# Kernel tuning notes

Hardware: AMD Instinct MI355X
Metric: run time of the kernel (lower is better)

The kernel has to match this reference:

```python
import jax, jax.numpy as jnp
import numpy as np

N, D, H = 50000, 256, 8
HD = D // H
E = 800000
NEG_SLOPE = 0.2


def setup_inputs() -> dict:
    key = jax.random.key(0)
    ks = jax.random.split(key, 12)
    s = 1.0 / np.sqrt(D)
    return {
        "x": jax.random.normal(ks[0], (N, D), jnp.float32),
        "edge_index": jax.random.randint(ks[1], (2, E), 0, N, jnp.int64),
        "edge_attr": jax.random.normal(ks[2], (E, 16), jnp.float32),
        # GATConv params: lin weight (no bias), attention vectors, output bias
        "W": jax.random.normal(ks[3], (D, D), jnp.float32) * s,
        "att_src": jax.random.normal(ks[4], (H, HD), jnp.float32) * s,
        "att_dst": jax.random.normal(ks[5], (H, HD), jnp.float32) * s,
        "bias": jnp.zeros((D,), jnp.float32),
        # LayerNorm
        "ln_g": jnp.ones((D,), jnp.float32),
        "ln_b": jnp.zeros((D,), jnp.float32),
        # FFN
        "W1": jax.random.normal(ks[6], (D, D), jnp.float32) * s,
        "b1": jnp.zeros((D,), jnp.float32),
        "W2": jax.random.normal(ks[7], (D, D), jnp.float32) * s,
        "b2": jnp.zeros((D,), jnp.float32),
    }


def _gat_layer(x, edge_index, W, att_src, att_dst, bias, ln_g, ln_b, W1, b1, W2, b2):
    n = x.shape[0]
    # GATConv default add_self_loops=True
    sl = jnp.arange(n, dtype=edge_index.dtype)
    src = jnp.concatenate([edge_index[0], sl])  # [E+N]
    dst = jnp.concatenate([edge_index[1], sl])  # [E+N]

    xp = (x @ W).reshape(n, H, HD)                      # [N,H,hd]
    a_src = jnp.einsum("nhd,hd->nh", xp, att_src)        # [N,H]
    a_dst = jnp.einsum("nhd,hd->nh", xp, att_dst)        # [N,H]

    e = a_src[src] + a_dst[dst]                          # [E+N,H]
    e = jax.nn.leaky_relu(e, NEG_SLOPE)
    # segment softmax over destination nodes (every node has a self loop)
    m = jax.ops.segment_max(e, dst, num_segments=n)      # [N,H]
    ex = jnp.exp(e - m[dst])
    denom = jax.ops.segment_sum(ex, dst, num_segments=n) # [N,H]
    alpha = ex / (denom[dst] + 1e-16)                    # [E+N,H]

    msg = alpha[:, :, None] * xp[src]                    # [E+N,H,hd]
    out = jax.ops.segment_sum(msg, dst, num_segments=n)  # [N,H,hd]
    h = out.reshape(n, D) + bias

    # residual + LayerNorm
    r = h + x
    mu = jnp.mean(r, axis=-1, keepdims=True)
    var = jnp.mean(jnp.square(r - mu), axis=-1, keepdims=True)
    hn = (r - mu) / jnp.sqrt(var + 1e-5) * ln_g + ln_b

    # FFN
    return jax.nn.relu(hn @ W1 + b1) @ W2 + b2


def reference(x, edge_index, edge_attr, W, att_src, att_dst, bias, ln_g, ln_b, W1, b1, W2, b2):
    # edge_attr is accepted but unused (GATConv built without edge_dim)
    return _gat_layer(x, edge_index, W, att_src, att_dst, bias, ln_g, ln_b, W1, b1, W2, b2)
```

## Files before the change

### kernel.cpp

```cpp
#include <hip/hip_runtime.h>
#include <hip/hip_bf16.h>

#define H 8
#define HD 32
#define DD 256
#define NEG_SLOPE 0.2f

typedef short bf16x8 __attribute__((ext_vector_type(8)));
typedef float f32x4 __attribute__((ext_vector_type(4)));

__device__ __forceinline__ unsigned short f2bf(float f) {
    unsigned int u = __float_as_uint(f);
    unsigned int r = (u + 0x7fffu + ((u >> 16) & 1u)) >> 16;
    return (unsigned short)r;
}
__device__ __forceinline__ float bf2f(unsigned short b) {
    return __uint_as_float(((unsigned int)b) << 16);
}

#define GLOAD_LDS16(g, s)                                                        \
    __builtin_amdgcn_global_load_lds((const __attribute__((address_space(1))) void*)(g), \
                                     (__attribute__((address_space(3))) void*)(s), 16, 0, 0)

__global__ __launch_bounds__(256) void prep(const float* __restrict__ x, unsigned short* __restrict__ xb,
                                            const float* __restrict__ W, unsigned short* __restrict__ Wt,
                                            const float* __restrict__ W1, unsigned short* __restrict__ W1t,
                                            const float* __restrict__ W2, unsigned short* __restrict__ W2t,
                                            int* __restrict__ cnt, int N, int n4, int ZB) {
    int b = blockIdx.x;
    int tid = threadIdx.x;
    if (b < 768) {
        const float* src = (b < 256) ? W : (b < 512) ? W1 : W2;
        unsigned short* dst = (b < 256) ? Wt : (b < 512) ? W1t : W2t;
        int i = (b & 255) * 256 + tid;
        int n = i >> 8, k = i & 255;
        dst[i] = f2bf(src[k * 256 + n]);
    } else if (b < 768 + ZB) {
        int i = (b - 768) * 256 + tid;
        if (i < N) cnt[i] = 0;
    } else {
        int i = (b - 768 - ZB) * 256 + tid;
        if (i < n4) {
            float4 v = ((const float4*)x)[i];
            ushort4 o;
            o.x = f2bf(v.x); o.y = f2bf(v.y); o.z = f2bf(v.z); o.w = f2bf(v.w);
            ((ushort4*)xb)[i] = o;
        }
    }
}

template <bool ATTN, bool PHASE2>
__global__ __launch_bounds__(256) void gemm_fused(
    const unsigned short* __restrict__ A,
    const unsigned short* __restrict__ B1t, const float* __restrict__ b1,
    const unsigned short* __restrict__ B2t, const float* __restrict__ b2,
    void* __restrict__ Cout, int M,
    const float* __restrict__ att_s, const float* __restrict__ att_d,
    float* __restrict__ a_srcO, float* __restrict__ a_dstO) {
    __shared__ __align__(16) unsigned short Als[4096];
    __shared__ __align__(16) unsigned short Bls[16384];
    __shared__ __align__(16) unsigned short t1ls[PHASE2 ? 64 * 280 : 8];

    const int tid = threadIdx.x;
    const int l = tid & 63;
    const int w = tid >> 6;
    const int r16 = l & 15, q0 = l >> 4;
    const int row0 = blockIdx.x * 64;

    const int ca0 = w * 128 + l, ca1 = ca0 + 64;
    const unsigned short* gA0 = A + (size_t)min(row0 + (ca0 & 63), M - 1) * DD + (ca0 >> 6) * 8;
    const unsigned short* gA1 = A + (size_t)min(row0 + (ca1 & 63), M - 1) * DD + (ca1 >> 6) * 8;
    unsigned short* lA0 = &Als[ca0 * 8];
    unsigned short* lA1 = &Als[ca1 * 8];

    const unsigned short* gB[8];
    unsigned short* lB[8];
#pragma unroll
    for (int k = 0; k < 8; k++) {
        int c = w * 512 + k * 64 + l;
        gB[k] = B1t + (size_t)(c & 255) * DD + (c >> 8) * 8;
        lB[k] = &Bls[c * 8];
    }

    f32x4 zero = {0.f, 0.f, 0.f, 0.f};
    f32x4 acc[4][4];
#pragma unroll
    for (int i = 0; i < 4; i++)
#pragma unroll
        for (int j = 0; j < 4; j++) acc[i][j] = zero;

    for (int kk = 0; kk < 256; kk += 64) {
        GLOAD_LDS16(gA0 + kk, lA0);
        GLOAD_LDS16(gA1 + kk, lA1);
#pragma unroll
        for (int k = 0; k < 8; k++) GLOAD_LDS16(gB[k] + kk, lB[k]);
        __syncthreads();
#pragma unroll
        for (int t = 0; t < 2; t++) {
            int q = t * 4 + q0;
            bf16x8 af[4], bf[4];
#pragma unroll
            for (int i = 0; i < 4; i++)
                af[i] = *(const bf16x8*)&Als[(q * 64 + i * 16 + r16) * 8];
#pragma unroll
            for (int j = 0; j < 4; j++)
                bf[j] = *(const bf16x8*)&Bls[(q * 256 + w * 64 + j * 16 + r16) * 8];
#pragma unroll
            for (int i = 0; i < 4; i++)
#pragma unroll
                for (int j = 0; j < 4; j++)
                    acc[i][j] = __builtin_amdgcn_mfma_f32_16x16x32_bf16(af[i], bf[j], acc[i][j], 0, 0, 0);
        }
        __syncthreads();
    }

    if (!PHASE2) {
        float aws0, aws1, aws2, aws3, awd0, awd1, awd2, awd3;
        int hA = 0, hB = 0;
        if (ATTN) {
            hA = w * 2; hB = hA + 1;
            aws0 = att_s[hA * HD + r16];
            aws1 = att_s[hA * HD + 16 + r16];
            aws2 = att_s[hB * HD + r16];
            aws3 = att_s[hB * HD + 16 + r16];
            awd0 = att_d[hA * HD + r16];
            awd1 = att_d[hA * HD + 16 + r16];
            awd2 = att_d[hB * HD + r16];
            awd3 = att_d[hB * HD + 16 + r16];
        }
#pragma unroll
        for (int i = 0; i < 4; i++) {
#pragma unroll
            for (int r = 0; r < 4; r++) {
                int row = row0 + i * 16 + q0 * 4 + r;
                if (row < M) {
#pragma unroll
                    for (int j = 0; j < 4; j++) {
                        int col = w * 64 + j * 16 + r16;
                        ((unsigned short*)Cout)[(size_t)row * DD + col] = f2bf(acc[i][j][r]);
                    }
                }
                if (ATTN) {
                    float v0 = acc[i][0][r], v1 = acc[i][1][r];
                    float v2 = acc[i][2][r], v3 = acc[i][3][r];
                    float ps0 = v0 * aws0 + v1 * aws1;
                    float ps1 = v2 * aws2 + v3 * aws3;
                    float pd0 = v0 * awd0 + v1 * awd1;
                    float pd1 = v2 * awd2 + v3 * awd3;
#pragma unroll
                    for (int m = 1; m < 16; m <<= 1) {
                        ps0 += __shfl_xor(ps0, m, 64);
                        ps1 += __shfl_xor(ps1, m, 64);
                        pd0 += __shfl_xor(pd0, m, 64);
                        pd1 += __shfl_xor(pd1, m, 64);
                    }
                    if (r16 == 0 && row < M) {
                        a_srcO[row * H + hA] = ps0;
                        a_srcO[row * H + hB] = ps1;
                        a_dstO[row * H + hA] = pd0;
                        a_dstO[row * H + hB] = pd1;
                    }
                }
            }
        }
    } else {
        float bb1[4];
#pragma unroll
        for (int j = 0; j < 4; j++) bb1[j] = b1[w * 64 + j * 16 + r16];
#pragma unroll
        for (int i = 0; i < 4; i++)
#pragma unroll
            for (int r = 0; r < 4; r++) {
                int rl = i * 16 + q0 * 4 + r;
#pragma unroll
                for (int j = 0; j < 4; j++) {
                    float v = fmaxf(acc[i][j][r] + bb1[j], 0.f);
                    t1ls[rl * 280 + w * 64 + j * 16 + r16] = f2bf(v);
                }
            }
        __syncthreads();

        const unsigned short* gB2[8];
#pragma unroll
        for (int k = 0; k < 8; k++) {
            int c = w * 512 + k * 64 + l;
            gB2[k] = B2t + (size_t)(c & 255) * DD + (c >> 8) * 8;
        }
#pragma unroll
        for (int i = 0; i < 4; i++)
#pragma unroll
            for (int j = 0; j < 4; j++) acc[i][j] = zero;

        for (int kk = 0; kk < 256; kk += 64) {
#pragma unroll
            for (int k = 0; k < 8; k++) GLOAD_LDS16(gB2[k] + kk, lB[k]);
            __syncthreads();
#pragma unroll
            for (int t = 0; t < 2; t++) {
                int q = t * 4 + q0;
                bf16x8 af[4], bf[4];
#pragma unroll
                for (int i = 0; i < 4; i++)
                    af[i] = *(const bf16x8*)&t1ls[(i * 16 + r16) * 280 + kk + q * 8];
#pragma unroll
                for (int j = 0; j < 4; j++)
                    bf[j] = *(const bf16x8*)&Bls[(q * 256 + w * 64 + j * 16 + r16) * 8];
#pragma unroll
                for (int i = 0; i < 4; i++)
#pragma unroll
                    for (int j = 0; j < 4; j++)
                        acc[i][j] = __builtin_amdgcn_mfma_f32_16x16x32_bf16(af[i], bf[j], acc[i][j], 0, 0, 0);
            }
            __syncthreads();
        }

        float bb2[4];
#pragma unroll
        for (int j = 0; j < 4; j++) bb2[j] = b2[w * 64 + j * 16 + r16];
#pragma unroll
        for (int i = 0; i < 4; i++)
#pragma unroll
            for (int r = 0; r < 4; r++) {
                int row = row0 + i * 16 + q0 * 4 + r;
                if (row < M) {
#pragma unroll
                    for (int j = 0; j < 4; j++) {
                        int col = w * 64 + j * 16 + r16;
                        ((float*)Cout)[(size_t)row * DD + col] = acc[i][j][r] + bb2[j];
                    }
                }
            }
    }
}

__global__ void hist_kernel(const int* __restrict__ ei, int* __restrict__ counts, int E) {
    int e = blockIdx.x * blockDim.x + threadIdx.x;
    if (e < E) atomicAdd(&counts[ei[E + e]], 1);
}

__global__ __launch_bounds__(1024) void scan_block(const int* __restrict__ cnt,
                                                   int* __restrict__ row_ptr,
                                                   int* __restrict__ bsum, int N) {
    __shared__ int ws[16];
    int i = blockIdx.x * 1024 + threadIdx.x;
    int lane = threadIdx.x & 63, w = threadIdx.x >> 6;
    int v = (i < N) ? cnt[i] : 0;
    int sv = v;
#pragma unroll
    for (int off = 1; off < 64; off <<= 1) {
        int t = __shfl_up(sv, off, 64);
        if (lane >= off) sv += t;
    }
    if (lane == 63) ws[w] = sv;
    __syncthreads();
    if (w == 0) {
        int s = (lane < 16) ? ws[lane] : 0;
#pragma unroll
        for (int off = 1; off < 16; off <<= 1) {
            int t = __shfl_up(s, off, 64);
            if (lane >= off) s += t;
        }
        if (lane < 16) ws[lane] = s;
    }
    __syncthreads();
    int incl = sv + ((w > 0) ? ws[w - 1] : 0);
    if (i < N) row_ptr[i + 1] = incl;
    if (threadIdx.x == 1023) bsum[blockIdx.x] = incl;
}

__global__ void scan_partial(int* __restrict__ bsum, int nb) {
    int lane = threadIdx.x;
    int v = (lane < nb) ? bsum[lane] : 0;
    int s = v;
#pragma unroll
    for (int off = 1; off < 64; off <<= 1) {
        int t = __shfl_up(s, off, 64);
        if (lane >= off) s += t;
    }
    if (lane < nb) bsum[lane] = s - v;
}

__global__ __launch_bounds__(1024) void scan_add(int* __restrict__ row_ptr,
                                                 const int* __restrict__ bsum, int N) {
    int i = blockIdx.x * 1024 + threadIdx.x;
    if (i == 0) row_ptr[0] = 0;
    if (i < N) row_ptr[i + 1] += bsum[blockIdx.x];
}

__global__ void scatter_kernel(const int* __restrict__ ei, int* __restrict__ row_ptr,
                               int* __restrict__ src_sorted, int E) {
    int e = blockIdx.x * blockDim.x + threadIdx.x;
    if (e >= E) return;
    int s = ei[e];
    int d = ei[E + e];
    int pos = atomicAdd(&row_ptr[d], 1);
    src_sorted[pos] = s;
}

__global__ __launch_bounds__(256) void aggregate_ln(
    const unsigned short* __restrict__ xp, const unsigned short* __restrict__ x_bf,
    const float* __restrict__ a_src, const float* __restrict__ a_dst,
    const int* __restrict__ rp, const int* __restrict__ src_sorted,
    const float* __restrict__ bias, const float* __restrict__ ln_g,
    const float* __restrict__ ln_b, unsigned short* __restrict__ hn, int N) {
    int wave = threadIdx.x >> 6;
    int lane = threadIdx.x & 63;
    int n = blockIdx.x * 4 + wave;
    if (n >= N) return;
    int h = lane >> 3;

    float adst = a_dst[n * H + h];
    float e0 = a_src[n * H + h] + adst;
    e0 = (e0 > 0.f) ? e0 : NEG_SLOPE * e0;
    float ex = __expf(e0);
    ushort4 u = *(const ushort4*)(xp + (size_t)n * DD + lane * 4);
    float acc0 = ex * bf2f(u.x), acc1 = ex * bf2f(u.y);
    float acc2 = ex * bf2f(u.z), acc3 = ex * bf2f(u.w);
    float denom = ex;

    int beg = (n > 0) ? rp[n - 1] : 0;
    int end = rp[n];
    int i = beg;
    for (; i + 7 < end; i += 8) {
        int s[8];
        float es[8];
        ushort4 uu[8];
#pragma unroll
        for (int k = 0; k < 8; k++) s[k] = src_sorted[i + k];
#pragma unroll
        for (int k = 0; k < 8; k++) es[k] = a_src[s[k] * H + h];
#pragma unroll
        for (int k = 0; k < 8; k++) uu[k] = *(const ushort4*)(xp + (size_t)s[k] * DD + lane * 4);
#pragma unroll
        for (int k = 0; k < 8; k++) {
            float e = es[k] + adst;
            e = (e > 0.f) ? e : NEG_SLOPE * e;
            float wk = __expf(e);
            acc0 += wk * bf2f(uu[k].x);
            acc1 += wk * bf2f(uu[k].y);
            acc2 += wk * bf2f(uu[k].z);
            acc3 += wk * bf2f(uu[k].w);
            denom += wk;
        }
    }
    for (; i < end; i++) {
        int s0 = src_sorted[i];
        float es0 = a_src[s0 * H + h];
        ushort4 u0 = *(const ushort4*)(xp + (size_t)s0 * DD + lane * 4);
        float e0a = es0 + adst;
        e0a = (e0a > 0.f) ? e0a : NEG_SLOPE * e0a;
        float w0 = __expf(e0a);
        acc0 += w0 * bf2f(u0.x);
        acc1 += w0 * bf2f(u0.y);
        acc2 += w0 * bf2f(u0.z);
        acc3 += w0 * bf2f(u0.w);
        denom += w0;
    }
    float inv = 1.f / (denom + 1e-16f);
    float4 bb = *(const float4*)(bias + lane * 4);
    ushort4 xr = *(const ushort4*)(x_bf + (size_t)n * DD + lane * 4);
    float r0 = acc0 * inv + bb.x + bf2f(xr.x);
    float r1 = acc1 * inv + bb.y + bf2f(xr.y);
    float r2 = acc2 * inv + bb.z + bf2f(xr.z);
    float r3 = acc3 * inv + bb.w + bf2f(xr.w);

    float s = r0 + r1 + r2 + r3;
#pragma unroll
    for (int m = 1; m < 64; m <<= 1) s += __shfl_xor(s, m, 64);
    float mu = s * (1.f / 256.f);
    float d0 = r0 - mu, d1 = r1 - mu, d2 = r2 - mu, d3 = r3 - mu;
    float qv = d0 * d0 + d1 * d1 + d2 * d2 + d3 * d3;
#pragma unroll
    for (int m = 1; m < 64; m <<= 1) qv += __shfl_xor(qv, m, 64);
    float rstd = rsqrtf(qv * (1.f / 256.f) + 1e-5f);
    float4 g = *(const float4*)(ln_g + lane * 4);
    float4 b = *(const float4*)(ln_b + lane * 4);
    ushort4 o;
    o.x = f2bf(d0 * rstd * g.x + b.x);
    o.y = f2bf(d1 * rstd * g.y + b.y);
    o.z = f2bf(d2 * rstd * g.z + b.z);
    o.w = f2bf(d3 * rstd * g.w + b.w);
    *(ushort4*)(hn + (size_t)n * DD + lane * 4) = o;
}

extern "C" void kernel_launch(void* const* d_in, const int* in_sizes, int n_in,
                              void* d_out, int out_size, void* d_ws, size_t ws_size,
                              hipStream_t stream) {
    const float* x = (const float*)d_in[0];
    const int* edge_index = (const int*)d_in[1];
    const float* W = (const float*)d_in[3];
    const float* att_src = (const float*)d_in[4];
    const float* att_dst = (const float*)d_in[5];
    const float* bias = (const float*)d_in[6];
    const float* ln_g = (const float*)d_in[7];
    const float* ln_b = (const float*)d_in[8];
    const float* W1 = (const float*)d_in[9];
    const float* b1 = (const float*)d_in[10];
    const float* W2 = (const float*)d_in[11];
    const float* b2 = (const float*)d_in[12];

    const int N = in_sizes[0] / DD;
    const int E = in_sizes[1] / 2;

    char* p = (char*)d_ws;
    auto carve = [&](size_t bytes) {
        char* r = p;
        p += (bytes + 255) & ~(size_t)255;
        return r;
    };
    unsigned short* x_bf = (unsigned short*)carve((size_t)N * DD * 2);
    unsigned short* xp_bf = (unsigned short*)carve((size_t)N * DD * 2);
    unsigned short* hn_bf = (unsigned short*)carve((size_t)N * DD * 2);
    float* a_src = (float*)carve((size_t)N * H * 4);
    float* a_dst = (float*)carve((size_t)N * H * 4);
    int* row_ptr = (int*)carve((size_t)(N + 1) * 4);
    int* cnt = (int*)carve((size_t)N * 4);
    int* bsum = (int*)carve(256 * 4);
    int* src_sorted = (int*)carve((size_t)E * 4);
    unsigned short* Wt = (unsigned short*)carve(65536 * 2);
    unsigned short* W1t = (unsigned short*)carve(65536 * 2);
    unsigned short* W2t = (unsigned short*)carve(65536 * 2);

    const int n4 = N * DD / 4;
    const int ZB = (N + 255) / 256;

    int prep_blocks = 768 + ZB + (n4 + 255) / 256;
    prep<<<prep_blocks, 256, 0, stream>>>(x, x_bf, W, Wt, W1, W1t, W2, W2t, cnt, N, n4, ZB);

    const int gblocks = (N + 63) / 64;

    gemm_fused<true, false><<<gblocks, 256, 0, stream>>>(
        x_bf, Wt, nullptr, nullptr, nullptr, xp_bf, N, att_src, att_dst, a_src, a_dst);

    hist_kernel<<<(E + 255) / 256, 256, 0, stream>>>(edge_index, cnt, E);
    int nb = (N + 1023) / 1024;
    scan_block<<<nb, 1024, 0, stream>>>(cnt, row_ptr, bsum, N);
    scan_partial<<<1, 64, 0, stream>>>(bsum, nb);
    scan_add<<<nb, 1024, 0, stream>>>(row_ptr, bsum, N);
    scatter_kernel<<<(E + 255) / 256, 256, 0, stream>>>(edge_index, row_ptr, src_sorted, E);

    aggregate_ln<<<(N + 3) / 4, 256, 0, stream>>>(xp_bf, x_bf, a_src, a_dst, row_ptr, src_sorted,
                                                  bias, ln_g, ln_b, hn_bf, N);

    gemm_fused<false, true><<<gblocks, 256, 0, stream>>>(
        hn_bf, W1t, b1, W2t, b2, d_out, N, nullptr, nullptr, nullptr, nullptr);
}
```

Before: 396.8 us.

## Fuse CSR build into prep and GEMM kernels using per-edge ranks

The histogram now runs inside the prep kernel and records each edge's atomic rank within its destination. The scatter becomes a plain write at row_ptr[d]+rank, carried out by extra blocks appended to the first GEMM launch. The separate partial-scan kernel is folded into scan_add, which sums the block totals itself. This removes several kernel launches and the second pass of atomics, at the cost of an extra rank array in memory and a separate zeroing kernel.

```diff
diff --git a/kernel.cpp b/kernel.cpp
--- a/kernel.cpp
+++ b/kernel.cpp
@@ -22,11 +22,17 @@
     __builtin_amdgcn_global_load_lds((const __attribute__((address_space(1))) void*)(g), \
                                      (__attribute__((address_space(3))) void*)(s), 16, 0, 0)
 
+__global__ __launch_bounds__(256) void zero_cnt(int* __restrict__ cnt, int N) {
+    int i = blockIdx.x * 256 + threadIdx.x;
+    if (i < N) cnt[i] = 0;
+}
+
 __global__ __launch_bounds__(256) void prep(const float* __restrict__ x, unsigned short* __restrict__ xb,
                                             const float* __restrict__ W, unsigned short* __restrict__ Wt,
                                             const float* __restrict__ W1, unsigned short* __restrict__ W1t,
                                             const float* __restrict__ W2, unsigned short* __restrict__ W2t,
-                                            int* __restrict__ cnt, int N, int n4, int ZB) {
+                                            const int* __restrict__ ei, int* __restrict__ rank,
+                                            int* __restrict__ cnt, int N, int n4, int E, int HB) {
     int b = blockIdx.x;
     int tid = threadIdx.x;
     if (b < 768) {
@@ -35,11 +41,11 @@
         int i = (b & 255) * 256 + tid;
         int n = i >> 8, k = i & 255;
         dst[i] = f2bf(src[k * 256 + n]);
-    } else if (b < 768 + ZB) {
-        int i = (b - 768) * 256 + tid;
-        if (i < N) cnt[i] = 0;
+    } else if (b < 768 + HB) {
+        int e = (b - 768) * 256 + tid;
+        if (e < E) rank[e] = atomicAdd(&cnt[ei[E + e]], 1);
     } else {
-        int i = (b - 768 - ZB) * 256 + tid;
+        int i = (b - 768 - HB) * 256 + tid;
         if (i < n4) {
             float4 v = ((const float4*)x)[i];
             ushort4 o;
@@ -56,12 +62,27 @@
     const unsigned short* __restrict__ B2t, const float* __restrict__ b2,
     void* __restrict__ Cout, int M,
     const float* __restrict__ att_s, const float* __restrict__ att_d,
-    float* __restrict__ a_srcO, float* __restrict__ a_dstO) {
+    float* __restrict__ a_srcO, float* __restrict__ a_dstO,
+    const int* __restrict__ ei, const int* __restrict__ rank,
+    const int* __restrict__ rp, int* __restrict__ src_sorted, int E, int gB) {
     __shared__ __align__(16) unsigned short Als[4096];
     __shared__ __align__(16) unsigned short Bls[16384];
     __shared__ __align__(16) unsigned short t1ls[PHASE2 ? 64 * 280 : 8];
 
     const int tid = threadIdx.x;
+
+    if constexpr (ATTN) {
+        if ((int)blockIdx.x >= gB) {
+            int e = ((int)blockIdx.x - gB) * 256 + tid;
+            if (e < E) {
+                int s = ei[e];
+                int d = ei[E + e];
+                src_sorted[rp[d] + rank[e]] = s;
+            }
+            return;
+        }
+    }
+
     const int l = tid & 63;
     const int w = tid >> 6;
     const int r16 = l & 15, q0 = l >> 4;
@@ -73,12 +94,12 @@
     unsigned short* lA0 = &Als[ca0 * 8];
     unsigned short* lA1 = &Als[ca1 * 8];
 
-    const unsigned short* gB[8];
+    const unsigned short* gB8[8];
     unsigned short* lB[8];
 #pragma unroll
     for (int k = 0; k < 8; k++) {
         int c = w * 512 + k * 64 + l;
-        gB[k] = B1t + (size_t)(c & 255) * DD + (c >> 8) * 8;
+        gB8[k] = B1t + (size_t)(c & 255) * DD + (c >> 8) * 8;
         lB[k] = &Bls[c * 8];
     }
 
@@ -93,7 +114,7 @@
         GLOAD_LDS16(gA0 + kk, lA0);
         GLOAD_LDS16(gA1 + kk, lA1);
 #pragma unroll
-        for (int k = 0; k < 8; k++) GLOAD_LDS16(gB[k] + kk, lB[k]);
+        for (int k = 0; k < 8; k++) GLOAD_LDS16(gB8[k] + kk, lB[k]);
         __syncthreads();
 #pragma unroll
         for (int t = 0; t < 2; t++) {
@@ -233,11 +254,6 @@
     }
 }
 
-__global__ void hist_kernel(const int* __restrict__ ei, int* __restrict__ counts, int E) {
-    int e = blockIdx.x * blockDim.x + threadIdx.x;
-    if (e < E) atomicAdd(&counts[ei[E + e]], 1);
-}
-
 __global__ __launch_bounds__(1024) void scan_block(const int* __restrict__ cnt,
                                                    int* __restrict__ row_ptr,
                                                    int* __restrict__ bsum, int N) {
@@ -268,33 +284,22 @@
     if (threadIdx.x == 1023) bsum[blockIdx.x] = incl;
 }
 
-__global__ void scan_partial(int* __restrict__ bsum, int nb) {
-    int lane = threadIdx.x;
-    int v = (lane < nb) ? bsum[lane] : 0;
-    int s = v;
-#pragma unroll
-    for (int off = 1; off < 64; off <<= 1) {
-        int t = __shfl_up(s, off, 64);
-        if (lane >= off) s += t;
-    }
-    if (lane < nb) bsum[lane] = s - v;
-}
-
 __global__ __launch_bounds__(1024) void scan_add(int* __restrict__ row_ptr,
                                                  const int* __restrict__ bsum, int N) {
-    int i = blockIdx.x * 1024 + threadIdx.x;
+    __shared__ int offs;
+    int b = blockIdx.x;
+    if (threadIdx.x < 64) {
+        int lane = threadIdx.x;
+        int s = 0;
+        for (int j = lane; j < b; j += 64) s += bsum[j];
+#pragma unroll
+        for (int m = 1; m < 64; m <<= 1) s += __shfl_xor(s, m, 64);
+        if (lane == 0) offs = s;
+    }
+    __syncthreads();
+    int i = b * 1024 + threadIdx.x;
     if (i == 0) row_ptr[0] = 0;
-    if (i < N) row_ptr[i + 1] += bsum[blockIdx.x];
-}
-
-__global__ void scatter_kernel(const int* __restrict__ ei, int* __restrict__ row_ptr,
-                               int* __restrict__ src_sorted, int E) {
-    int e = blockIdx.x * blockDim.x + threadIdx.x;
-    if (e >= E) return;
-    int s = ei[e];
-    int d = ei[E + e];
-    int pos = atomicAdd(&row_ptr[d], 1);
-    src_sorted[pos] = s;
+    if (i < N) row_ptr[i + 1] += offs;
 }
 
 __global__ __launch_bounds__(256) void aggregate_ln(
@@ -318,8 +323,8 @@
     float acc2 = ex * bf2f(u.z), acc3 = ex * bf2f(u.w);
     float denom = ex;
 
-    int beg = (n > 0) ? rp[n - 1] : 0;
-    int end = rp[n];
+    int beg = rp[n];
+    int end = rp[n + 1];
     int i = beg;
     for (; i + 7 < end; i += 8) {
         int s[8];
@@ -417,31 +422,34 @@
     int* cnt = (int*)carve((size_t)N * 4);
     int* bsum = (int*)carve(256 * 4);
     int* src_sorted = (int*)carve((size_t)E * 4);
+    int* rank = (int*)carve((size_t)E * 4);
     unsigned short* Wt = (unsigned short*)carve(65536 * 2);
     unsigned short* W1t = (unsigned short*)carve(65536 * 2);
     unsigned short* W2t = (unsigned short*)carve(65536 * 2);
 
     const int n4 = N * DD / 4;
-    const int ZB = (N + 255) / 256;
-
-    int prep_blocks = 768 + ZB + (n4 + 255) / 256;
-    prep<<<prep_blocks, 256, 0, stream>>>(x, x_bf, W, Wt, W1, W1t, W2, W2t, cnt, N, n4, ZB);
-
-    const int gblocks = (N + 63) / 64;
-
-    gemm_fused<true, false><<<gblocks, 256, 0, stream>>>(
-        x_bf, Wt, nullptr, nullptr, nullptr, xp_bf, N, att_src, att_dst, a_src, a_dst);
-
-    hist_kernel<<<(E + 255) / 256, 256, 0, stream>>>(edge_index, cnt, E);
+    const int HB = (E + 255) / 256;
+
+    zero_cnt<<<(N + 255) / 256, 256, 0, stream>>>(cnt, N);
+
+    int prep_blocks = 768 + HB + (n4 + 255) / 256;
+    prep<<<prep_blocks, 256, 0, stream>>>(x, x_bf, W, Wt, W1, W1t, W2, W2t,
+                                          edge_index, rank, cnt, N, n4, E, HB);
+
     int nb = (N + 1023) / 1024;
     scan_block<<<nb, 1024, 0, stream>>>(cnt, row_ptr, bsum, N);
-    scan_partial<<<1, 64, 0, stream>>>(bsum, nb);
     scan_add<<<nb, 1024, 0, stream>>>(row_ptr, bsum, N);
-    scatter_kernel<<<(E + 255) / 256, 256, 0, stream>>>(edge_index, row_ptr, src_sorted, E);
+
+    const int gblocks = (N + 63) / 64;
+
+    gemm_fused<true, false><<<gblocks + HB, 256, 0, stream>>>(
+        x_bf, Wt, nullptr, nullptr, nullptr, xp_bf, N, att_src, att_dst, a_src, a_dst,
+        edge_index, rank, row_ptr, src_sorted, E, gblocks);
 
     aggregate_ln<<<(N + 3) / 4, 256, 0, stream>>>(xp_bf, x_bf, a_src, a_dst, row_ptr, src_sorted,
                                                   bias, ln_g, ln_b, hn_bf, N);
 
     gemm_fused<false, true><<<gblocks, 256, 0, stream>>>(
-        hn_bf, W1t, b1, W2t, b2, d_out, N, nullptr, nullptr, nullptr, nullptr);
-}
+        hn_bf, W1t, b1, W2t, b2, d_out, N, nullptr, nullptr, nullptr, nullptr,
+        nullptr, nullptr, nullptr, nullptr, 0, gblocks);
+}
```

After: 349.8 us. -11.8%, faster.
